# Optimization experiments

Measured on AMD Instinct MI355X. Metric: run time of the kernel, lower is better.

Reference implementation:

```python
import jax, jax.numpy as jnp
import numpy as np

B, N, DIM = 2, 192, 512
HEADS, DH = 8, 64  # key_value_heads == heads, dim_head_values == dim_head
KV_SETS = 2
SPLIT = (HEADS * DH, KV_SETS * HEADS * DH, KV_SETS * HEADS * DH)


def rmsnorm(x, w):
    # torch.nn.RMSNorm with eps=None uses finfo(dtype).eps
    eps = jnp.asarray(jnp.finfo(x.dtype).eps, x.dtype)
    var = jnp.mean(jnp.square(x), axis=-1, keepdims=True)
    return x * jax.lax.rsqrt(var + eps) * w


def two_simplicial_attend(q, k1, k2, v1, v2):
    scale = q.shape[-1] ** -0.5
    # trilinear scores over both key sets: [b h i j k]
    sim = jnp.einsum('bhid,bhjd,bhkd->bhijk', q, k1, k2) * scale
    b, h, i, j, k = sim.shape
    attn = jax.nn.softmax(sim.reshape(b, h, i, j * k), axis=-1).reshape(b, h, i, j, k)
    return jnp.einsum('bhijk,bhjd,bhkd->bhid', attn, v1, v2)


def setup_inputs() -> dict:
    key = jax.random.key(0)
    ks = jax.random.split(key, 8)
    tokens = jax.random.normal(ks[0], (B, N, DIM), dtype=jnp.float32)
    w_qkv = jax.random.normal(ks[1], (sum(SPLIT), DIM), dtype=jnp.float32) * 0.02
    w_out = jax.random.normal(ks[2], (DIM, HEADS * DH), dtype=jnp.float32) * 0.02
    q_norm_w = jnp.ones((DH,), jnp.float32)
    k1_norm_w = jnp.ones((DH,), jnp.float32)
    k2_norm_w = jnp.ones((DH,), jnp.float32)
    v1_norm_w = jnp.ones((DH,), jnp.float32)
    v2_norm_w = jnp.ones((DH,), jnp.float32)
    return {
        'tokens': tokens, 'w_qkv': w_qkv, 'w_out': w_out,
        'q_norm_w': q_norm_w, 'k1_norm_w': k1_norm_w, 'k2_norm_w': k2_norm_w,
        'v1_norm_w': v1_norm_w, 'v2_norm_w': v2_norm_w,
    }


def reference(tokens, w_qkv, w_out, q_norm_w, k1_norm_w, k2_norm_w, v1_norm_w, v2_norm_w):
    b, n, _ = tokens.shape
    qkv = tokens @ w_qkv.T
    q, kcat, vcat = jnp.split(qkv, [SPLIT[0], SPLIT[0] + SPLIT[1]], axis=-1)
    # 'b n (h d) -> b h n d' with h=heads; k/v carry kv_sets*dh per head, chunked last
    q = q.reshape(b, n, HEADS, DH).transpose(0, 2, 1, 3)
    kcat = kcat.reshape(b, n, HEADS, KV_SETS * DH).transpose(0, 2, 1, 3)
    vcat = vcat.reshape(b, n, HEADS, KV_SETS * DH).transpose(0, 2, 1, 3)
    k1, k2 = kcat[..., :DH], kcat[..., DH:]
    v1, v2 = vcat[..., :DH], vcat[..., DH:]
    q = rmsnorm(q, q_norm_w)
    k1 = rmsnorm(k1, k1_norm_w)
    k2 = rmsnorm(k2, k2_norm_w)
    v1 = rmsnorm(v1, v1_norm_w)
    v2 = rmsnorm(v2, v2_norm_w)
    out = two_simplicial_attend(q, k1, k2, v1, v2)  # [b h n dh]
    out = out.transpose(0, 2, 1, 3).reshape(b, n, HEADS * DH)
    return out @ w_out.T
```

## Files before the change

kernel.cpp:

```cpp
#include <hip/hip_runtime.h>

#define B_ 2
#define N_ 192
#define DIM_ 512
#define H_ 8
#define DH_ 64
#define EPS_RMS 1.1920929e-7f
#define QSC 0.18033688011112042f
#define ARR_ (B_*H_*N_*DH_)

typedef float v4f __attribute__((ext_vector_type(4)));
typedef short v8s __attribute__((ext_vector_type(8)));

__device__ __forceinline__ unsigned int cvtpk(float a, float b) {
  unsigned int d;
  asm("v_cvt_pk_bf16_f32 %0, %1, %2" : "=v"(d) : "v"(a), "v"(b));
  return d;
}
__device__ __forceinline__ float bf16_lo(unsigned int u) { return __uint_as_float(u << 16); }
__device__ __forceinline__ float bf16_hi(unsigned int u) { return __uint_as_float(u & 0xffff0000u); }

#if __has_builtin(__builtin_amdgcn_exp2f)
__device__ __forceinline__ float fexp2(float x) { return __builtin_amdgcn_exp2f(x); }
#else
__device__ __forceinline__ float fexp2(float x) {
  float r; asm("v_exp_f32 %0, %1" : "=v"(r) : "v"(x)); return r;
}
#endif

__device__ __forceinline__ v4f mfma16(uint4 a, uint4 b, v4f c) {
  union { uint4 u; v8s s; } ua, ub;
  ua.u = a; ub.u = b;
  return __builtin_amdgcn_mfma_f32_16x16x32_bf16(ua.s, ub.s, c, 0, 0, 0);
}

__device__ __forceinline__ void split8(const float* s, uint4& hi, uint4& lo) {
  float4 f0 = *(const float4*)s;
  float4 f1 = *(const float4*)(s + 4);
  hi.x = cvtpk(f0.x, f0.y); hi.y = cvtpk(f0.z, f0.w);
  hi.z = cvtpk(f1.x, f1.y); hi.w = cvtpk(f1.z, f1.w);
  lo.x = cvtpk(f0.x - bf16_lo(hi.x), f0.y - bf16_hi(hi.x));
  lo.y = cvtpk(f0.z - bf16_lo(hi.y), f0.w - bf16_hi(hi.y));
  lo.z = cvtpk(f1.x - bf16_lo(hi.z), f1.y - bf16_hi(hi.z));
  lo.w = cvtpk(f1.z - bf16_lo(hi.w), f1.w - bf16_hi(hi.w));
}

__global__ __launch_bounds__(256, 2)
void qkv_mfma_kernel(const float* __restrict__ tokens, const float* __restrict__ w_qkv,
                     const float* __restrict__ qw, const float* __restrict__ k1w,
                     const float* __restrict__ k2w, const float* __restrict__ v1w,
                     const float* __restrict__ v2w,
                     float* __restrict__ Q, float* __restrict__ K1, float* __restrict__ K2,
                     float* __restrict__ V1, float* __restrict__ V2)
{
  const int bn = blockIdx.x;
  const int bm = blockIdx.y;
  const int tid = threadIdx.x;
  const int w = tid >> 6, l = tid & 63;
  const int c = l & 15, q = l >> 4;
  const int mhalf = w & 1, nhalf = w >> 1;

  __shared__ __align__(16) uint4 Ahi[8*32], Alo[8*32];
  __shared__ __align__(16) uint4 Bhi[8*64], Blo[8*64];
  __shared__ float red[32][2];

  v4f acc[2] = {(v4f){0,0,0,0}, (v4f){0,0,0,0}};

  for (int kc = 0; kc < 8; ++kc) {
    const int k0 = kc * 64;
    {
      int m = tid >> 3, g = tid & 7;
      uint4 hi, lo;
      split8(tokens + (size_t)(bm*32 + m)*DIM_ + k0 + g*8, hi, lo);
      Ahi[g*32 + (m ^ g)] = hi;
      Alo[g*32 + (m ^ g)] = lo;
    }
    #pragma unroll
    for (int cc = 0; cc < 2; ++cc) {
      int e = tid + 256*cc;
      int n = e >> 3, g = e & 7;
      uint4 hi, lo;
      split8(w_qkv + (size_t)(bn*64 + n)*DIM_ + k0 + g*8, hi, lo);
      Bhi[g*64 + (n ^ g)] = hi;
      Blo[g*64 + (n ^ g)] = lo;
    }
    __syncthreads();
    #pragma unroll
    for (int kh = 0; kh < 2; ++kh) {
      int g = kh*4 + q;
      int m = mhalf*16 + c;
      uint4 ah = Ahi[g*32 + (m ^ g)];
      uint4 al = Alo[g*32 + (m ^ g)];
      #pragma unroll
      for (int nt = 0; nt < 2; ++nt) {
        int n = nhalf*32 + nt*16 + c;
        uint4 bh = Bhi[g*64 + (n ^ g)];
        uint4 bl = Blo[g*64 + (n ^ g)];
        acc[nt] = mfma16(ah, bh, acc[nt]);
        acc[nt] = mfma16(ah, bl, acc[nt]);
        acc[nt] = mfma16(al, bh, acc[nt]);
      }
    }
    __syncthreads();
  }

  float ss[4];
  #pragma unroll
  for (int r = 0; r < 4; ++r) {
    ss[r] = acc[0][r]*acc[0][r] + acc[1][r]*acc[1][r];
    #pragma unroll
    for (int off = 1; off < 16; off <<= 1) ss[r] += __shfl_xor(ss[r], off, 64);
  }
  if (c == 0) {
    #pragma unroll
    for (int r = 0; r < 4; ++r) red[mhalf*16 + q*4 + r][nhalf] = ss[r];
  }
  __syncthreads();

  const float* nw; float* dst; int hh;
  if (bn < 8)       { nw = qw; dst = Q; hh = bn; }
  else if (bn < 24) { int g = bn - 8;  hh = g >> 1; nw = (g & 1) ? k2w : k1w; dst = (g & 1) ? K2 : K1; }
  else              { int g = bn - 24; hh = g >> 1; nw = (g & 1) ? v2w : v1w; dst = (g & 1) ? V2 : V1; }

  #pragma unroll
  for (int r = 0; r < 4; ++r) {
    int row = mhalf*16 + q*4 + r;
    float sst = red[row][0] + red[row][1];
    float sc = rsqrtf(sst * (1.0f/64.0f) + EPS_RMS);
    int m = bm*32 + row;
    int b = (m >= N_) ? 1 : 0;
    int n = m - b*N_;
    size_t obase = (((size_t)(b*H_ + hh))*N_ + n)*DH_;
    #pragma unroll
    for (int nt = 0; nt < 2; ++nt) {
      int d = nhalf*32 + nt*16 + c;
      dst[obase + d] = acc[nt][r] * sc * nw[d];
    }
  }
}

__global__ __launch_bounds__(256, 2)
void attn_kernel(const float* __restrict__ Qg, const float* __restrict__ K1g,
                 const float* __restrict__ K2g, const float* __restrict__ V1g,
                 const float* __restrict__ V2g, float* __restrict__ ATT)
{
  __shared__ __align__(16) unsigned char lds[64032];
  uint4* K2B  = (uint4*)(lds);
  uint4* V2B  = (uint4*)(lds + 24576);
  float* qS   = (float*)(lds + 61440);
  float* redF = (float*)(lds + 62976);
  float* redL = (float*)(lds + 64000);

  const int tid = threadIdx.x;
  const int w = tid >> 6, l = tid & 63;
  const int c = l & 15, q = l >> 4;
  const int bh = blockIdx.x >> 5;
  const int sub = blockIdx.x & 31;
  const int b = bh >> 3, h = bh & 7;
  const int i0 = sub * 6;
  const size_t base = (size_t)bh * (N_ * DH_);

  for (int t = tid; t < 24*64; t += 256) {
    int blk = t >> 6, ll = t & 63;
    int nt = blk >> 1, ks = blk & 1;
    int kcol = nt*16 + (ll & 15);
    int d0 = ks*32 + ((ll >> 4) << 3);
    const float* s = K2g + base + kcol*64 + d0;
    float4 f0 = *(const float4*)s;
    float4 f1 = *(const float4*)(s + 4);
    uint4 wv;
    wv.x = cvtpk(f0.x, f0.y); wv.y = cvtpk(f0.z, f0.w);
    wv.z = cvtpk(f1.x, f1.y); wv.w = cvtpk(f1.z, f1.w);
    K2B[t] = wv;
  }
  for (int t = tid; t < 24*64; t += 256) {
    int blk = t >> 6, ll = t & 63;
    int nt = blk / 6, ks = blk % 6;
    int d = nt*16 + (ll & 15);
    int kc0 = ks*32 + ((ll >> 4) << 3);
    const float* s = V2g + base + kc0*64 + d;
    uint4 wv;
    wv.x = cvtpk(s[0],   s[64]);
    wv.y = cvtpk(s[128], s[192]);
    wv.z = cvtpk(s[256], s[320]);
    wv.w = cvtpk(s[384], s[448]);
    V2B[t] = wv;
  }
  for (int t = tid; t < 6*64; t += 256)
    qS[t] = Qg[base + (size_t)(i0 + (t >> 6))*64 + (t & 63)] * QSC;

  unsigned int k1p[6][4];
  #pragma unroll
  for (int jt = 0; jt < 3; ++jt)
    #pragma unroll
    for (int ks = 0; ks < 2; ++ks) {
      int j = w*48 + jt*16 + c;
      int d0 = ks*32 + (q << 3);
      const float* s = K1g + base + j*64 + d0;
      float4 f0 = *(const float4*)s;
      float4 f1 = *(const float4*)(s + 4);
      k1p[jt*2+ks][0] = cvtpk(f0.x, f0.y);
      k1p[jt*2+ks][1] = cvtpk(f0.z, f0.w);
      k1p[jt*2+ks][2] = cvtpk(f1.x, f1.y);
      k1p[jt*2+ks][3] = cvtpk(f1.z, f1.w);
    }
  unsigned int v1p[12][2];
  #pragma unroll
  for (int jt = 0; jt < 3; ++jt)
    #pragma unroll
    for (int dt = 0; dt < 4; ++dt) {
      int jb = w*48 + jt*16 + q*4;
      int d = dt*16 + c;
      const float* s = V1g + base + jb*64 + d;
      v1p[jt*4+dt][0] = cvtpk(s[0],   s[64]);
      v1p[jt*4+dt][1] = cvtpk(s[128], s[192]);
    }

  __syncthreads();

  unsigned char* Pw = lds + 49152 + w*3072;
  const int rs = l ^ (l >> 4);

  for (int ii = 0; ii < 6; ++ii) {
    float qv[2][8];
    #pragma unroll
    for (int ks = 0; ks < 2; ++ks) {
      const float* s = qS + ii*64 + ks*32 + (q << 3);
      float4 a = *(const float4*)s;
      float4 bq = *(const float4*)(s + 4);
      qv[ks][0]=a.x; qv[ks][1]=a.y; qv[ks][2]=a.z; qv[ks][3]=a.w;
      qv[ks][4]=bq.x; qv[ks][5]=bq.y; qv[ks][6]=bq.z; qv[ks][7]=bq.w;
    }
    uint4 afr[3][2];
    #pragma unroll
    for (int jt = 0; jt < 3; ++jt)
      #pragma unroll
      for (int ks = 0; ks < 2; ++ks) {
        unsigned int wds[4];
        #pragma unroll
        for (int e = 0; e < 4; ++e) {
          float lo = bf16_lo(k1p[jt*2+ks][e]) * qv[ks][2*e];
          float hi = bf16_hi(k1p[jt*2+ks][e]) * qv[ks][2*e+1];
          wds[e] = cvtpk(lo, hi);
        }
        afr[jt][ks].x = wds[0]; afr[jt][ks].y = wds[1];
        afr[jt][ks].z = wds[2]; afr[jt][ks].w = wds[3];
      }

    v4f racc[3][4];
    #pragma unroll
    for (int jt = 0; jt < 3; ++jt)
      #pragma unroll
      for (int dt = 0; dt < 4; ++dt)
        racc[jt][dt] = (v4f){0.f, 0.f, 0.f, 0.f};
    float psum = 0.f;

    for (int ch = 0; ch < 6; ++ch) {
      uint4 kb[2][2];
      #pragma unroll
      for (int ktl = 0; ktl < 2; ++ktl)
        #pragma unroll
        for (int ks = 0; ks < 2; ++ks)
          kb[ktl][ks] = K2B[((ch*2 + ktl)*2 + ks)*64 + l];

      v4f sacc[3][2];
      #pragma unroll
      for (int jt = 0; jt < 3; ++jt)
        #pragma unroll
        for (int ktl = 0; ktl < 2; ++ktl) {
          v4f z = (v4f){0.f, 0.f, 0.f, 0.f};
          z = mfma16(afr[jt][0], kb[ktl][0], z);
          z = mfma16(afr[jt][1], kb[ktl][1], z);
          sacc[jt][ktl] = z;
        }

      #pragma unroll
      for (int jt = 0; jt < 3; ++jt)
        #pragma unroll
        for (int ktl = 0; ktl < 2; ++ktl) {
          int kc = ktl*16 + c;
          int kc3 = kc >> 3;
          #pragma unroll
          for (int r = 0; r < 4; ++r) {
            float p = fexp2(sacc[jt][ktl][r]);
            psum += p;
            int slot = kc3*16 + q*4 + r;
            slot ^= (slot >> 4);
            *(unsigned short*)(Pw + jt*1024 + slot*16 + ((kc & 7) << 1)) =
                (unsigned short)cvtpk(p, p);
          }
        }

      uint4 pa[3];
      #pragma unroll
      for (int jt = 0; jt < 3; ++jt)
        pa[jt] = *(uint4*)(Pw + jt*1024 + rs*16);
      uint4 vb[4];
      #pragma unroll
      for (int dt = 0; dt < 4; ++dt)
        vb[dt] = V2B[(dt*6 + ch)*64 + l];
      #pragma unroll
      for (int jt = 0; jt < 3; ++jt)
        #pragma unroll
        for (int dt = 0; dt < 4; ++dt)
          racc[jt][dt] = mfma16(pa[jt], vb[dt], racc[jt][dt]);
    }

    float lsum = psum;
    #pragma unroll
    for (int off = 32; off; off >>= 1) lsum += __shfl_xor(lsum, off, 64);

    float op[4] = {0.f, 0.f, 0.f, 0.f};
    #pragma unroll
    for (int jt = 0; jt < 3; ++jt)
      #pragma unroll
      for (int dt = 0; dt < 4; ++dt) {
        op[dt] = fmaf(bf16_lo(v1p[jt*4+dt][0]), racc[jt][dt][0], op[dt]);
        op[dt] = fmaf(bf16_hi(v1p[jt*4+dt][0]), racc[jt][dt][1], op[dt]);
        op[dt] = fmaf(bf16_lo(v1p[jt*4+dt][1]), racc[jt][dt][2], op[dt]);
        op[dt] = fmaf(bf16_hi(v1p[jt*4+dt][1]), racc[jt][dt][3], op[dt]);
      }
    #pragma unroll
    for (int dt = 0; dt < 4; ++dt) {
      op[dt] += __shfl_xor(op[dt], 16, 64);
      op[dt] += __shfl_xor(op[dt], 32, 64);
    }
    if (l < 16) {
      #pragma unroll
      for (int dt = 0; dt < 4; ++dt) redF[w*64 + dt*16 + l] = op[dt];
    }
    if (l == 0) redL[w] = lsum;
    __syncthreads();
    if (tid < 64) {
      float o = redF[tid] + redF[64 + tid] + redF[128 + tid] + redF[192 + tid];
      float lt = redL[0] + redL[1] + redL[2] + redL[3];
      ATT[((size_t)(b*N_ + i0 + ii))*(H_*DH_) + h*64 + tid] = o / lt;
    }
    __syncthreads();
  }
}

__global__ __launch_bounds__(256, 2)
void out_proj_kernel(const float* __restrict__ ATT, const float* __restrict__ w_out,
                     float* __restrict__ out)
{
  const int bn = blockIdx.x;
  const int bm = blockIdx.y;
  const int tid = threadIdx.x;
  const int w = tid >> 6, l = tid & 63;
  const int c = l & 15, q = l >> 4;
  const int mhalf = w & 1, nhalf = w >> 1;

  __shared__ __align__(16) uint4 Ahi[8*32], Alo[8*32];
  __shared__ __align__(16) uint4 Bhi[8*64], Blo[8*64];

  v4f acc[2] = {(v4f){0,0,0,0}, (v4f){0,0,0,0}};

  for (int kc = 0; kc < 8; ++kc) {
    const int k0 = kc * 64;
    {
      int m = tid >> 3, g = tid & 7;
      uint4 hi, lo;
      split8(ATT + (size_t)(bm*32 + m)*DIM_ + k0 + g*8, hi, lo);
      Ahi[g*32 + (m ^ g)] = hi;
      Alo[g*32 + (m ^ g)] = lo;
    }
    #pragma unroll
    for (int cc = 0; cc < 2; ++cc) {
      int e = tid + 256*cc;
      int n = e >> 3, g = e & 7;
      uint4 hi, lo;
      split8(w_out + (size_t)(bn*64 + n)*DIM_ + k0 + g*8, hi, lo);
      Bhi[g*64 + (n ^ g)] = hi;
      Blo[g*64 + (n ^ g)] = lo;
    }
    __syncthreads();
    #pragma unroll
    for (int kh = 0; kh < 2; ++kh) {
      int g = kh*4 + q;
      int m = mhalf*16 + c;
      uint4 ah = Ahi[g*32 + (m ^ g)];
      uint4 al = Alo[g*32 + (m ^ g)];
      #pragma unroll
      for (int nt = 0; nt < 2; ++nt) {
        int n = nhalf*32 + nt*16 + c;
        uint4 bh = Bhi[g*64 + (n ^ g)];
        uint4 bl = Blo[g*64 + (n ^ g)];
        acc[nt] = mfma16(ah, bh, acc[nt]);
        acc[nt] = mfma16(ah, bl, acc[nt]);
        acc[nt] = mfma16(al, bh, acc[nt]);
      }
    }
    __syncthreads();
  }

  #pragma unroll
  for (int r = 0; r < 4; ++r) {
    int m = bm*32 + mhalf*16 + q*4 + r;
    #pragma unroll
    for (int nt = 0; nt < 2; ++nt) {
      int d = nhalf*32 + nt*16 + c;
      out[(size_t)m*DIM_ + bn*64 + d] = acc[nt][r];
    }
  }
}

extern "C" void kernel_launch(void* const* d_in, const int* in_sizes, int n_in,
                              void* d_out, int out_size, void* d_ws, size_t ws_size,
                              hipStream_t stream) {
  const float* tokens = (const float*)d_in[0];
  const float* w_qkv  = (const float*)d_in[1];
  const float* w_out  = (const float*)d_in[2];
  const float* qw     = (const float*)d_in[3];
  const float* k1w    = (const float*)d_in[4];
  const float* k2w    = (const float*)d_in[5];
  const float* v1w    = (const float*)d_in[6];
  const float* v2w    = (const float*)d_in[7];
  float* out = (float*)d_out;

  float* ws  = (float*)d_ws;
  float* Q   = ws;
  float* K1  = ws + (size_t)ARR_;
  float* K2  = ws + (size_t)2*ARR_;
  float* V1  = ws + (size_t)3*ARR_;
  float* V2  = ws + (size_t)4*ARR_;
  float* ATT = ws + (size_t)5*ARR_;

  qkv_mfma_kernel<<<dim3(40, 12), 256, 0, stream>>>(tokens, w_qkv, qw, k1w, k2w, v1w, v2w,
                                                    Q, K1, K2, V1, V2);
  attn_kernel<<<dim3(512), 256, 0, stream>>>(Q, K1, K2, V1, V2, ATT);
  out_proj_kernel<<<dim3(8, 12), 256, 0, stream>>>(ATT, w_out, out);
}
```

Measured before the change: 139.5 us.

## Prepack bf16 operands, emit attention-ready K2/V2, shrink attention tile

Adds a prepack kernel that splits tokens into bf16 hi/lo planes once, in MFMA fragment order. The QKV kernel then reads A fragments straight from global memory and writes K2/V2 already bf16-packed in the attention layout. The attention kernel copies the prepacked K2/V2 into LDS without conversion, processes 4 queries per block over 768 blocks at occupancy 3, and reorders the score MFMA so each P tile is written and reused per j-tile in a smaller LDS buffer. Attention output is stored as bf16 hi/lo fragments so the out-projection skips its own split. The trade is an extra launch and uncached global fragment reads, plus more redundant K2/V2 staging across the larger number of attention blocks.

```diff
diff --git a/kernel.cpp b/kernel.cpp
--- a/kernel.cpp
+++ b/kernel.cpp
@@ -24,7 +24,7 @@
 __device__ __forceinline__ float fexp2(float x) { return __builtin_amdgcn_exp2f(x); }
 #else
 __device__ __forceinline__ float fexp2(float x) {
-  float r; asm("v_exp_f32 %0, %1" : "=v"(r) : "v"(x)); return r;
+  float r; asm("v_exp_f32 %0, %1\n\ts_nop 1" : "=v"(r) : "v"(x)); return r;
 }
 #endif
 
@@ -45,13 +45,29 @@
   lo.w = cvtpk(f1.z - bf16_lo(hi.w), f1.w - bf16_hi(hi.w));
 }
 
+__global__ __launch_bounds__(256)
+void prepack_kernel(const float* __restrict__ tokens,
+                    unsigned short* __restrict__ AtkHi, unsigned short* __restrict__ AtkLo)
+{
+  int idx = blockIdx.x * 256 + threadIdx.x;
+  int token = idx >> 6, grp = idx & 63;
+  int kc = grp >> 3, g = grp & 7;
+  const float* s = tokens + (size_t)token*DIM_ + kc*64 + g*8;
+  uint4 hi, lo; split8(s, hi, lo);
+  int o = (((token >> 5)*8 + kc)*8 + g)*32 + (token & 31);
+  ((uint4*)AtkHi)[o] = hi;
+  ((uint4*)AtkLo)[o] = lo;
+}
+
 __global__ __launch_bounds__(256, 2)
-void qkv_mfma_kernel(const float* __restrict__ tokens, const float* __restrict__ w_qkv,
+void qkv_mfma_kernel(const unsigned short* __restrict__ AtkHi,
+                     const unsigned short* __restrict__ AtkLo,
+                     const float* __restrict__ w_qkv,
                      const float* __restrict__ qw, const float* __restrict__ k1w,
                      const float* __restrict__ k2w, const float* __restrict__ v1w,
                      const float* __restrict__ v2w,
-                     float* __restrict__ Q, float* __restrict__ K1, float* __restrict__ K2,
-                     float* __restrict__ V1, float* __restrict__ V2)
+                     float* __restrict__ Q, float* __restrict__ K1, float* __restrict__ V1,
+                     uint4* __restrict__ K2P, uint4* __restrict__ V2P)
 {
   const int bn = blockIdx.x;
   const int bm = blockIdx.y;
@@ -60,21 +76,16 @@
   const int c = l & 15, q = l >> 4;
   const int mhalf = w & 1, nhalf = w >> 1;
 
-  __shared__ __align__(16) uint4 Ahi[8*32], Alo[8*32];
   __shared__ __align__(16) uint4 Bhi[8*64], Blo[8*64];
   __shared__ float red[32][2];
 
+  const uint4* AtkHiU = (const uint4*)AtkHi;
+  const uint4* AtkLoU = (const uint4*)AtkLo;
+
   v4f acc[2] = {(v4f){0,0,0,0}, (v4f){0,0,0,0}};
 
   for (int kc = 0; kc < 8; ++kc) {
     const int k0 = kc * 64;
-    {
-      int m = tid >> 3, g = tid & 7;
-      uint4 hi, lo;
-      split8(tokens + (size_t)(bm*32 + m)*DIM_ + k0 + g*8, hi, lo);
-      Ahi[g*32 + (m ^ g)] = hi;
-      Alo[g*32 + (m ^ g)] = lo;
-    }
     #pragma unroll
     for (int cc = 0; cc < 2; ++cc) {
       int e = tid + 256*cc;
@@ -88,9 +99,8 @@
     #pragma unroll
     for (int kh = 0; kh < 2; ++kh) {
       int g = kh*4 + q;
-      int m = mhalf*16 + c;
-      uint4 ah = Ahi[g*32 + (m ^ g)];
-      uint4 al = Alo[g*32 + (m ^ g)];
+      uint4 ah = AtkHiU[((bm*8 + kc)*8 + g)*32 + mhalf*16 + c];
+      uint4 al = AtkLoU[((bm*8 + kc)*8 + g)*32 + mhalf*16 + c];
       #pragma unroll
       for (int nt = 0; nt < 2; ++nt) {
         int n = nhalf*32 + nt*16 + c;
@@ -117,77 +127,101 @@
   }
   __syncthreads();
 
-  const float* nw; float* dst; int hh;
-  if (bn < 8)       { nw = qw; dst = Q; hh = bn; }
-  else if (bn < 24) { int g = bn - 8;  hh = g >> 1; nw = (g & 1) ? k2w : k1w; dst = (g & 1) ? K2 : K1; }
-  else              { int g = bn - 24; hh = g >> 1; nw = (g & 1) ? v2w : v1w; dst = (g & 1) ? V2 : V1; }
-
+  const float* nw; float* dstPlane = nullptr; int hh; bool isK2 = false, isV2 = false;
+  if (bn < 8)       { nw = qw; dstPlane = Q; hh = bn; }
+  else if (bn < 24) { int g = bn - 8;  hh = g >> 1;
+                      if (g & 1) { nw = k2w; isK2 = true; } else { nw = k1w; dstPlane = K1; } }
+  else              { int g = bn - 24; hh = g >> 1;
+                      if (g & 1) { nw = v2w; isV2 = true; } else { nw = v1w; dstPlane = V1; } }
+
+  const int b = (bm >= 6) ? 1 : 0;
+  const int bmm = bm - b*6;
+  const int bh = b*8 + hh;
+
+  float sc[4];
   #pragma unroll
   for (int r = 0; r < 4; ++r) {
     int row = mhalf*16 + q*4 + r;
     float sst = red[row][0] + red[row][1];
-    float sc = rsqrtf(sst * (1.0f/64.0f) + EPS_RMS);
-    int m = bm*32 + row;
-    int b = (m >= N_) ? 1 : 0;
-    int n = m - b*N_;
-    size_t obase = (((size_t)(b*H_ + hh))*N_ + n)*DH_;
-    #pragma unroll
-    for (int nt = 0; nt < 2; ++nt) {
-      int d = nhalf*32 + nt*16 + c;
-      dst[obase + d] = acc[nt][r] * sc * nw[d];
-    }
-  }
-}
-
-__global__ __launch_bounds__(256, 2)
+    sc[r] = rsqrtf(sst * (1.0f/64.0f) + EPS_RMS);
+  }
+
+  if (dstPlane) {
+    #pragma unroll
+    for (int r = 0; r < 4; ++r) {
+      int row = mhalf*16 + q*4 + r;
+      int n = bmm*32 + row;
+      size_t obase = (((size_t)bh)*N_ + n)*DH_;
+      #pragma unroll
+      for (int nt = 0; nt < 2; ++nt) {
+        int d = nhalf*32 + nt*16 + c;
+        dstPlane[obase + d] = acc[nt][r] * sc[r] * nw[d];
+      }
+    }
+  } else {
+    float* tile = (float*)Bhi;
+    #pragma unroll
+    for (int r = 0; r < 4; ++r) {
+      int row = mhalf*16 + q*4 + r;
+      #pragma unroll
+      for (int nt = 0; nt < 2; ++nt) {
+        int d = nhalf*32 + nt*16 + c;
+        tile[row*64 + d] = acc[nt][r] * sc[r] * nw[d];
+      }
+    }
+    __syncthreads();
+    if (isK2) {
+      int ntl = tid >> 7, ks2 = (tid >> 6) & 1, ll = tid & 63;
+      int tok = ntl*16 + (ll & 15);
+      int d0 = ks2*32 + ((ll >> 4) << 3);
+      const float* sp = tile + tok*64 + d0;
+      uint4 wv;
+      wv.x = cvtpk(sp[0], sp[1]); wv.y = cvtpk(sp[2], sp[3]);
+      wv.z = cvtpk(sp[4], sp[5]); wv.w = cvtpk(sp[6], sp[7]);
+      K2P[(size_t)bh*1536 + ((bmm*2 + ntl)*2 + ks2)*64 + ll] = wv;
+    } else {
+      int ntd = tid >> 6, ll = tid & 63;
+      int dd = ntd*16 + (ll & 15);
+      int t0 = (ll >> 4) << 3;
+      uint4 wv;
+      wv.x = cvtpk(tile[(t0+0)*64 + dd], tile[(t0+1)*64 + dd]);
+      wv.y = cvtpk(tile[(t0+2)*64 + dd], tile[(t0+3)*64 + dd]);
+      wv.z = cvtpk(tile[(t0+4)*64 + dd], tile[(t0+5)*64 + dd]);
+      wv.w = cvtpk(tile[(t0+6)*64 + dd], tile[(t0+7)*64 + dd]);
+      V2P[(size_t)bh*1536 + (ntd*6 + bmm)*64 + ll] = wv;
+    }
+  }
+}
+
+__global__ __launch_bounds__(256, 3)
 void attn_kernel(const float* __restrict__ Qg, const float* __restrict__ K1g,
-                 const float* __restrict__ K2g, const float* __restrict__ V1g,
-                 const float* __restrict__ V2g, float* __restrict__ ATT)
+                 const float* __restrict__ V1g,
+                 const uint4* __restrict__ K2P, const uint4* __restrict__ V2P,
+                 unsigned short* __restrict__ ATThi, unsigned short* __restrict__ ATTlo)
 {
-  __shared__ __align__(16) unsigned char lds[64032];
+  __shared__ __align__(16) unsigned char lds[54272];
   uint4* K2B  = (uint4*)(lds);
   uint4* V2B  = (uint4*)(lds + 24576);
-  float* qS   = (float*)(lds + 61440);
-  float* redF = (float*)(lds + 62976);
-  float* redL = (float*)(lds + 64000);
+  float* redF = (float*)(lds + 53248);
 
   const int tid = threadIdx.x;
   const int w = tid >> 6, l = tid & 63;
   const int c = l & 15, q = l >> 4;
-  const int bh = blockIdx.x >> 5;
-  const int sub = blockIdx.x & 31;
+  const int bid = blockIdx.x;
+  const int bh = bid / 48;
+  const int sub = bid - bh*48;
   const int b = bh >> 3, h = bh & 7;
-  const int i0 = sub * 6;
+  const int i0 = sub * 4;
   const size_t base = (size_t)bh * (N_ * DH_);
 
-  for (int t = tid; t < 24*64; t += 256) {
-    int blk = t >> 6, ll = t & 63;
-    int nt = blk >> 1, ks = blk & 1;
-    int kcol = nt*16 + (ll & 15);
-    int d0 = ks*32 + ((ll >> 4) << 3);
-    const float* s = K2g + base + kcol*64 + d0;
-    float4 f0 = *(const float4*)s;
-    float4 f1 = *(const float4*)(s + 4);
-    uint4 wv;
-    wv.x = cvtpk(f0.x, f0.y); wv.y = cvtpk(f0.z, f0.w);
-    wv.z = cvtpk(f1.x, f1.y); wv.w = cvtpk(f1.z, f1.w);
-    K2B[t] = wv;
-  }
-  for (int t = tid; t < 24*64; t += 256) {
-    int blk = t >> 6, ll = t & 63;
-    int nt = blk / 6, ks = blk % 6;
-    int d = nt*16 + (ll & 15);
-    int kc0 = ks*32 + ((ll >> 4) << 3);
-    const float* s = V2g + base + kc0*64 + d;
-    uint4 wv;
-    wv.x = cvtpk(s[0],   s[64]);
-    wv.y = cvtpk(s[128], s[192]);
-    wv.z = cvtpk(s[256], s[320]);
-    wv.w = cvtpk(s[384], s[448]);
-    V2B[t] = wv;
-  }
-  for (int t = tid; t < 6*64; t += 256)
-    qS[t] = Qg[base + (size_t)(i0 + (t >> 6))*64 + (t & 63)] * QSC;
+  {
+    const uint4* s2 = K2P + (size_t)bh*1536;
+    const uint4* s3 = V2P + (size_t)bh*1536;
+    #pragma unroll
+    for (int t = 0; t < 6; ++t) K2B[tid + 256*t] = s2[tid + 256*t];
+    #pragma unroll
+    for (int t = 0; t < 6; ++t) V2B[tid + 256*t] = s3[tid + 256*t];
+  }
 
   unsigned int k1p[6][4];
   #pragma unroll
@@ -196,7 +230,7 @@
     for (int ks = 0; ks < 2; ++ks) {
       int j = w*48 + jt*16 + c;
       int d0 = ks*32 + (q << 3);
-      const float* s = K1g + base + j*64 + d0;
+      const float* s = K1g + base + (size_t)j*64 + d0;
       float4 f0 = *(const float4*)s;
       float4 f1 = *(const float4*)(s + 4);
       k1p[jt*2+ks][0] = cvtpk(f0.x, f0.y);
@@ -211,25 +245,25 @@
     for (int dt = 0; dt < 4; ++dt) {
       int jb = w*48 + jt*16 + q*4;
       int d = dt*16 + c;
-      const float* s = V1g + base + jb*64 + d;
+      const float* s = V1g + base + (size_t)jb*64 + d;
       v1p[jt*4+dt][0] = cvtpk(s[0],   s[64]);
       v1p[jt*4+dt][1] = cvtpk(s[128], s[192]);
     }
 
   __syncthreads();
 
-  unsigned char* Pw = lds + 49152 + w*3072;
-  const int rs = l ^ (l >> 4);
-
-  for (int ii = 0; ii < 6; ++ii) {
+  unsigned char* Pw = lds + 49152 + w*1024;
+  const int wG = (q ^ (c & 3)) << 4;
+
+  for (int ii = 0; ii < 4; ++ii) {
     float qv[2][8];
     #pragma unroll
     for (int ks = 0; ks < 2; ++ks) {
-      const float* s = qS + ii*64 + ks*32 + (q << 3);
+      const float* s = Qg + base + (size_t)(i0 + ii)*64 + ks*32 + (q << 3);
       float4 a = *(const float4*)s;
       float4 bq = *(const float4*)(s + 4);
-      qv[ks][0]=a.x; qv[ks][1]=a.y; qv[ks][2]=a.z; qv[ks][3]=a.w;
-      qv[ks][4]=bq.x; qv[ks][5]=bq.y; qv[ks][6]=bq.z; qv[ks][7]=bq.w;
+      qv[ks][0]=a.x*QSC;  qv[ks][1]=a.y*QSC;  qv[ks][2]=a.z*QSC;  qv[ks][3]=a.w*QSC;
+      qv[ks][4]=bq.x*QSC; qv[ks][5]=bq.y*QSC; qv[ks][6]=bq.z*QSC; qv[ks][7]=bq.w*QSC;
     }
     uint4 afr[3][2];
     #pragma unroll
@@ -258,52 +292,33 @@
     for (int ch = 0; ch < 6; ++ch) {
       uint4 kb[2][2];
       #pragma unroll
-      for (int ktl = 0; ktl < 2; ++ktl)
+      for (int mt = 0; mt < 2; ++mt)
         #pragma unroll
         for (int ks = 0; ks < 2; ++ks)
-          kb[ktl][ks] = K2B[((ch*2 + ktl)*2 + ks)*64 + l];
-
-      v4f sacc[3][2];
-      #pragma unroll
-      for (int jt = 0; jt < 3; ++jt)
-        #pragma unroll
-        for (int ktl = 0; ktl < 2; ++ktl) {
-          v4f z = (v4f){0.f, 0.f, 0.f, 0.f};
-          z = mfma16(afr[jt][0], kb[ktl][0], z);
-          z = mfma16(afr[jt][1], kb[ktl][1], z);
-          sacc[jt][ktl] = z;
-        }
-
-      #pragma unroll
-      for (int jt = 0; jt < 3; ++jt)
-        #pragma unroll
-        for (int ktl = 0; ktl < 2; ++ktl) {
-          int kc = ktl*16 + c;
-          int kc3 = kc >> 3;
-          #pragma unroll
-          for (int r = 0; r < 4; ++r) {
-            float p = fexp2(sacc[jt][ktl][r]);
-            psum += p;
-            int slot = kc3*16 + q*4 + r;
-            slot ^= (slot >> 4);
-            *(unsigned short*)(Pw + jt*1024 + slot*16 + ((kc & 7) << 1)) =
-                (unsigned short)cvtpk(p, p);
-          }
-        }
-
-      uint4 pa[3];
-      #pragma unroll
-      for (int jt = 0; jt < 3; ++jt)
-        pa[jt] = *(uint4*)(Pw + jt*1024 + rs*16);
+          kb[mt][ks] = K2B[((ch*2 + mt)*2 + ks)*64 + l];
       uint4 vb[4];
       #pragma unroll
       for (int dt = 0; dt < 4; ++dt)
         vb[dt] = V2B[(dt*6 + ch)*64 + l];
-      #pragma unroll
-      for (int jt = 0; jt < 3; ++jt)
+
+      #pragma unroll
+      for (int jt = 0; jt < 3; ++jt) {
+        #pragma unroll
+        for (int mt = 0; mt < 2; ++mt) {
+          v4f z = (v4f){0.f, 0.f, 0.f, 0.f};
+          z = mfma16(kb[mt][0], afr[jt][0], z);
+          z = mfma16(kb[mt][1], afr[jt][1], z);
+          float p0 = fexp2(z[0]), p1 = fexp2(z[1]), p2 = fexp2(z[2]), p3 = fexp2(z[3]);
+          psum += (p0 + p1) + (p2 + p3);
+          uint2 pwv; pwv.x = cvtpk(p0, p1); pwv.y = cvtpk(p2, p3);
+          int G = ((mt*2 + (q >> 1)) ^ (c & 3)) << 4;
+          *(uint2*)(Pw + c*64 + G + ((q & 1) << 3)) = pwv;
+        }
+        uint4 pa = *(uint4*)(Pw + c*64 + wG);
         #pragma unroll
         for (int dt = 0; dt < 4; ++dt)
-          racc[jt][dt] = mfma16(pa[jt], vb[dt], racc[jt][dt]);
+          racc[jt][dt] = mfma16(pa, vb[dt], racc[jt][dt]);
+      }
     }
 
     float lsum = psum;
@@ -329,20 +344,30 @@
       #pragma unroll
       for (int dt = 0; dt < 4; ++dt) redF[w*64 + dt*16 + l] = op[dt];
     }
-    if (l == 0) redL[w] = lsum;
+    if (l == 0) *(float*)(lds + 49152 + w*1024) = lsum;
     __syncthreads();
     if (tid < 64) {
       float o = redF[tid] + redF[64 + tid] + redF[128 + tid] + redF[192 + tid];
-      float lt = redL[0] + redL[1] + redL[2] + redL[3];
-      ATT[((size_t)(b*N_ + i0 + ii))*(H_*DH_) + h*64 + tid] = o / lt;
+      float lt = *(float*)(lds + 49152) + *(float*)(lds + 49152 + 1024)
+               + *(float*)(lds + 49152 + 2048) + *(float*)(lds + 49152 + 3072);
+      float v = o / lt;
+      int m_tok = b*N_ + i0 + ii;
+      int mt = m_tok >> 5, mloc = m_tok & 31;
+      int g = tid >> 3, e = tid & 7;
+      int off = ((((mt*8 + h)*8 + g)*32 + mloc) << 3) + e;
+      unsigned short hs = (unsigned short)cvtpk(v, v);
+      float resid = v - __uint_as_float(((unsigned int)hs) << 16);
+      unsigned short lsb = (unsigned short)cvtpk(resid, resid);
+      ATThi[off] = hs; ATTlo[off] = lsb;
     }
     __syncthreads();
   }
 }
 
 __global__ __launch_bounds__(256, 2)
-void out_proj_kernel(const float* __restrict__ ATT, const float* __restrict__ w_out,
-                     float* __restrict__ out)
+void out_proj_kernel(const unsigned short* __restrict__ ATThi,
+                     const unsigned short* __restrict__ ATTlo,
+                     const float* __restrict__ w_out, float* __restrict__ out)
 {
   const int bn = blockIdx.x;
   const int bm = blockIdx.y;
@@ -351,20 +376,15 @@
   const int c = l & 15, q = l >> 4;
   const int mhalf = w & 1, nhalf = w >> 1;
 
-  __shared__ __align__(16) uint4 Ahi[8*32], Alo[8*32];
   __shared__ __align__(16) uint4 Bhi[8*64], Blo[8*64];
+
+  const uint4* AHi = (const uint4*)ATThi;
+  const uint4* ALo = (const uint4*)ATTlo;
 
   v4f acc[2] = {(v4f){0,0,0,0}, (v4f){0,0,0,0}};
 
   for (int kc = 0; kc < 8; ++kc) {
     const int k0 = kc * 64;
-    {
-      int m = tid >> 3, g = tid & 7;
-      uint4 hi, lo;
-      split8(ATT + (size_t)(bm*32 + m)*DIM_ + k0 + g*8, hi, lo);
-      Ahi[g*32 + (m ^ g)] = hi;
-      Alo[g*32 + (m ^ g)] = lo;
-    }
     #pragma unroll
     for (int cc = 0; cc < 2; ++cc) {
       int e = tid + 256*cc;
@@ -378,9 +398,8 @@
     #pragma unroll
     for (int kh = 0; kh < 2; ++kh) {
       int g = kh*4 + q;
-      int m = mhalf*16 + c;
-      uint4 ah = Ahi[g*32 + (m ^ g)];
-      uint4 al = Alo[g*32 + (m ^ g)];
+      uint4 ah = AHi[((bm*8 + kc)*8 + g)*32 + mhalf*16 + c];
+      uint4 al = ALo[((bm*8 + kc)*8 + g)*32 + mhalf*16 + c];
       #pragma unroll
       for (int nt = 0; nt < 2; ++nt) {
         int n = nhalf*32 + nt*16 + c;
@@ -418,16 +437,21 @@
   const float* v2w    = (const float*)d_in[7];
   float* out = (float*)d_out;
 
-  float* ws  = (float*)d_ws;
+  float* ws = (float*)d_ws;
   float* Q   = ws;
   float* K1  = ws + (size_t)ARR_;
-  float* K2  = ws + (size_t)2*ARR_;
-  float* V1  = ws + (size_t)3*ARR_;
-  float* V2  = ws + (size_t)4*ARR_;
-  float* ATT = ws + (size_t)5*ARR_;
-
-  qkv_mfma_kernel<<<dim3(40, 12), 256, 0, stream>>>(tokens, w_qkv, qw, k1w, k2w, v1w, v2w,
-                                                    Q, K1, K2, V1, V2);
-  attn_kernel<<<dim3(512), 256, 0, stream>>>(Q, K1, K2, V1, V2, ATT);
-  out_proj_kernel<<<dim3(8, 12), 256, 0, stream>>>(ATT, w_out, out);
-}
+  float* V1  = ws + (size_t)2*ARR_;
+  uint4* K2P = (uint4*)(ws + (size_t)3*ARR_);
+  uint4* V2P = (uint4*)(ws + (size_t)3*ARR_ + 98304);
+  unsigned short* AtkHi = (unsigned short*)(ws + (size_t)3*ARR_ + 2*98304);
+  unsigned short* AtkLo = (unsigned short*)(ws + (size_t)3*ARR_ + 3*98304);
+  unsigned short* ATThi = AtkHi;
+  unsigned short* ATTlo = AtkLo;
+
+  prepack_kernel<<<96, 256, 0, stream>>>(tokens, AtkHi, AtkLo);
+  qkv_mfma_kernel<<<dim3(40, 12), 256, 0, stream>>>(AtkHi, AtkLo, w_qkv,
+                                                    qw, k1w, k2w, v1w, v2w,
+                                                    Q, K1, V1, K2P, V2P);
+  attn_kernel<<<768, 256, 0, stream>>>(Q, K1, V1, K2P, V2P, ATThi, ATTlo);
+  out_proj_kernel<<<dim3(8, 12), 256, 0, stream>>>(ATThi, ATTlo, w_out, out);
+}
```

Measured after the change: 242.6 us. 1.74x slower.
